# Kernel optimization log

Hardware: AMD Instinct MI355X
Metric: run time of the kernel (lower is better)

Reference implementation:

```python
import jax, jax.numpy as jnp
import numpy as np

N_NODES = 100000
N_EDGES = 1600000
IN_DIM = 128
HID = 128
OUT_DIM = 2
NUM_GRAPHS = 64
BN_EPS = 1e-5


def _glorot(key, shape):
    fan_in, fan_out = shape[0], shape[1]
    lim = np.sqrt(6.0 / (fan_in + fan_out))
    return jax.random.uniform(key, shape, jnp.float32, -lim, lim)


def setup_inputs() -> dict:
    key = jax.random.key(0)
    ks = jax.random.split(key, 12)
    x = jax.random.normal(ks[0], (N_NODES, IN_DIM), jnp.float32)
    edge_index = jax.random.randint(ks[1], (2, N_EDGES), 0, N_NODES, jnp.int64)
    batch = jnp.sort(jax.random.randint(ks[2], (N_NODES,), 0, NUM_GRAPHS, jnp.int64))
    return {
        "x": x,
        "edge_index": edge_index,
        "batch": batch,
        "W1": _glorot(ks[3], (IN_DIM, HID)), "b1": jnp.zeros((HID,), jnp.float32),
        "g1": jnp.ones((HID,), jnp.float32), "be1": jnp.zeros((HID,), jnp.float32),
        "W2": _glorot(ks[4], (HID, HID)), "b2": jnp.zeros((HID,), jnp.float32),
        "g2": jnp.ones((HID,), jnp.float32), "be2": jnp.zeros((HID,), jnp.float32),
        "Wc1": _glorot(ks[5], (HID, HID // 2)), "bc1": jnp.zeros((HID // 2,), jnp.float32),
        "Wc2": _glorot(ks[6], (HID // 2, OUT_DIM)), "bc2": jnp.zeros((OUT_DIM,), jnp.float32),
    }


def gcn_conv(x, src, dst, W, b):
    # PyG GCNConv: add self-loops, symmetric deg^{-1/2} normalization
    n = x.shape[0]
    loop = jnp.arange(n, dtype=src.dtype)
    s = jnp.concatenate([src, loop])
    d = jnp.concatenate([dst, loop])
    deg = jax.ops.segment_sum(jnp.ones_like(d, dtype=x.dtype), d, num_segments=n)
    dinv = jnp.where(deg > 0, jax.lax.rsqrt(deg), 0.0)
    xw = x @ W  # [N, out]
    msgs = xw[s] * (dinv[s] * dinv[d])[:, None]  # [E+N, out]
    out = jax.ops.segment_sum(msgs, d, num_segments=n)
    return out + b


def batchnorm(x, gamma, beta):
    mean = jnp.mean(x, axis=0)
    var = jnp.mean(jnp.square(x - mean), axis=0)  # biased, as torch BN
    return (x - mean) * jax.lax.rsqrt(var + BN_EPS) * gamma + beta


def reference(x, edge_index, batch, W1, b1, g1, be1, W2, b2, g2, be2, Wc1, bc1, Wc2, bc2):
    src, dst = edge_index[0], edge_index[1]
    x = jnp.nan_to_num(x, nan=0.0)
    # layer 1: GCNConv -> BN -> ReLU (dropout = identity in eval)
    h = jax.nn.relu(batchnorm(gcn_conv(x, src, dst, W1, b1), g1, be1))
    # layer 2
    h = jax.nn.relu(batchnorm(gcn_conv(h, src, dst, W2, b2), g2, be2))
    # global mean pool per graph
    sums = jax.ops.segment_sum(h, batch, num_segments=NUM_GRAPHS)
    counts = jax.ops.segment_sum(jnp.ones((h.shape[0],), h.dtype), batch, num_segments=NUM_GRAPHS)
    pooled = sums / jnp.maximum(counts, 1.0)[:, None]  # [G, HID]
    # classifier MLP
    z = jax.nn.relu(pooled @ Wc1 + bc1)
    out = z @ Wc2 + bc2
    return jnp.nan_to_num(out, nan=0.0)
```

## Files before the change

### kernel.cpp

```cpp
#include <hip/hip_runtime.h>

typedef unsigned int uint;
typedef unsigned short ushort;

#define HID 128
#define NGRAPH 64

typedef __attribute__((ext_vector_type(8))) short short8;
typedef __attribute__((ext_vector_type(4))) float floatx4;

__device__ __forceinline__ float bflo(uint w){ return __uint_as_float(w<<16); }
__device__ __forceinline__ float bfhi(uint w){ return __uint_as_float(w & 0xffff0000u); }
__device__ __forceinline__ float bf2f(ushort u){ return __uint_as_float(((uint)u)<<16); }
__device__ __forceinline__ ushort f2bf(float f){
  uint u = __float_as_uint(f);
  u = u + 0x7fffu + ((u>>16)&1u);
  return (ushort)(u>>16);
}
__device__ __forceinline__ uint pack2(float a, float b){
  return (uint)f2bf(a) | ((uint)f2bf(b)<<16);
}
__device__ __forceinline__ float nanz(float v){ return (v==v) ? v : 0.f; }

__device__ __forceinline__ int bat(const int* b, int i, int is64){
  return is64 ? b[2*(size_t)i] : b[i];
}

__global__ void k_zero_prep(int* __restrict__ cnt, float* __restrict__ stats1,
                            float* __restrict__ stats2, float* __restrict__ pooled,
                            uint* __restrict__ xwzero, int NN,
                            const int* __restrict__ ei, int* __restrict__ flags,
                            const float* __restrict__ W1, const float* __restrict__ W2,
                            ushort* __restrict__ wt1, ushort* __restrict__ wt2){
  int bid = blockIdx.x;
  if (bid < 512){
    int i = bid*256 + threadIdx.x;
    for (int t = i; t < NN; t += 512*256) cnt[t] = 0;
    if (i < 256){ stats1[i] = 0.f; stats2[i] = 0.f; }
    if (i < NGRAPH*HID) pooled[i] = 0.f;
    if (i < 64) xwzero[i] = 0u;
    if (bid == 0 && threadIdx.x < 64){
      int t = threadIdx.x;
      bool nz = (ei[2*t + 1] != 0) || (ei[2*(t+64) + 1] != 0);
      unsigned long long m = __ballot(nz);
      if (t == 0) flags[1] = (m == 0ULL) ? 1 : 0;
    }
  } else {
    int b = bid - 512;
    const float* W  = (b & 1) ? W2  : W1;
    ushort*      Wt = (b & 1) ? wt2 : wt1;
    int base = (b >> 1)*4096;
    for (int o = base + threadIdx.x; o < base + 4096; o += 256){
      int j    = o & 7;
      int lane = (o >> 3) & 63;
      int ct   = (o >> 9) & 7;
      int ks   = o >> 12;
      int k = ks*32 + (lane >> 4)*8 + j;
      int n = ct*16 + (lane & 15);
      Wt[o] = f2bf(W[(size_t)k*HID + n]);
    }
  }
}

__global__ void k_sentinel(ushort* out, int n){
  int i = blockIdx.x*blockDim.x + threadIdx.x;
  if (i < n) out[i] = 0x429A;
}


__global__ void k_hist(const int* __restrict__ ei, int* __restrict__ cnt, int E, int NN,
                       const int* __restrict__ flags){
  int is64 = flags[1];
  int e0 = (blockIdx.x*blockDim.x + threadIdx.x)*2;
  if (e0 >= E) return;
  bool h1 = (e0 + 1 < E);
  int d0, d1;
  if (is64){
    int4 v = *(const int4*)(ei + 2*(size_t)E + 2*(size_t)e0);
    d0 = v.x; d1 = v.z;
  } else {
    int2 v = *(const int2*)(ei + (size_t)E + e0);
    d0 = v.x; d1 = v.y;
  }
  if ((uint)d0 < (uint)NN) atomicAdd(&cnt[d0], 1);
  if (h1 && (uint)d1 < (uint)NN) atomicAdd(&cnt[d1], 1);
}

__global__ void k_scan1(const int* __restrict__ cnt, int* __restrict__ partials,
                        float* __restrict__ dinv, int NN){
  int t = threadIdx.x;
  int base = blockIdx.x*1024 + t*4;
  int v0=0,v1=0,v2=0,v3=0;
  if (base + 3 < NN){ int4 v = *(const int4*)(cnt + base); v0=v.x; v1=v.y; v2=v.z; v3=v.w; }
  else {
    if (base+0 < NN) v0 = cnt[base+0];
    if (base+1 < NN) v1 = cnt[base+1];
    if (base+2 < NN) v2 = cnt[base+2];
    if (base+3 < NN) v3 = cnt[base+3];
  }
  if (base+0 < NN) dinv[base+0] = rsqrtf((float)(v0+1));
  if (base+1 < NN) dinv[base+1] = rsqrtf((float)(v1+1));
  if (base+2 < NN) dinv[base+2] = rsqrtf((float)(v2+1));
  if (base+3 < NN) dinv[base+3] = rsqrtf((float)(v3+1));
  __shared__ int red[256];
  red[t] = v0+v1+v2+v3;
  __syncthreads();
  for (int off=128; off>0; off>>=1){
    if (t < off) red[t] += red[t+off];
    __syncthreads();
  }
  if (t==0) partials[blockIdx.x] = red[0];
}

__global__ void k_scan2(int* __restrict__ partials, int* __restrict__ offs, int npart, int NN){
  if (threadIdx.x==0 && blockIdx.x==0){
    int run = 0;
    for (int i=0;i<npart;i++){ int tt = partials[i]; partials[i] = run; run += tt; }
    offs[NN] = run;
  }
}

__global__ void k_scan3(const int* __restrict__ cnt, const int* __restrict__ partials,
                        int* __restrict__ offs, int* __restrict__ cursor, int NN){
  int t = threadIdx.x;
  int base = blockIdx.x*1024 + t*4;
  int v0=0,v1=0,v2=0,v3=0;
  if (base + 3 < NN){ int4 v = *(const int4*)(cnt + base); v0=v.x; v1=v.y; v2=v.z; v3=v.w; }
  else {
    if (base+0 < NN) v0 = cnt[base+0];
    if (base+1 < NN) v1 = cnt[base+1];
    if (base+2 < NN) v2 = cnt[base+2];
    if (base+3 < NN) v3 = cnt[base+3];
  }
  int tsum = v0+v1+v2+v3;
  __shared__ int sc[256];
  sc[t] = tsum;
  __syncthreads();
  for (int off=1; off<256; off<<=1){
    int val = (t >= off) ? sc[t-off] : 0;
    __syncthreads();
    sc[t] += val;
    __syncthreads();
  }
  int run = partials[blockIdx.x] + sc[t] - tsum;
  if (base+0 < NN){ offs[base+0] = run; cursor[base+0] = run; run += v0; }
  if (base+1 < NN){ offs[base+1] = run; cursor[base+1] = run; run += v1; }
  if (base+2 < NN){ offs[base+2] = run; cursor[base+2] = run; run += v2; }
  if (base+3 < NN){ offs[base+3] = run; cursor[base+3] = run; run += v3; }
}

__global__ void k_scatter(const int* __restrict__ ei, int* __restrict__ cursor,
                          int* __restrict__ srclist, int E, int NN,
                          const int* __restrict__ flags){
  int is64 = flags[1];
  int e0 = (blockIdx.x*blockDim.x + threadIdx.x)*2;
  if (e0 >= E) return;
  bool h1 = (e0 + 1 < E);
  int s0, s1, d0, d1;
  if (is64){
    int4 sv = *(const int4*)(ei + 2*(size_t)e0);
    int4 dv = *(const int4*)(ei + 2*(size_t)E + 2*(size_t)e0);
    s0 = sv.x; s1 = sv.z; d0 = dv.x; d1 = dv.z;
  } else {
    int2 sv = *(const int2*)(ei + (size_t)e0);
    int2 dv = *(const int2*)(ei + (size_t)E + e0);
    s0 = sv.x; s1 = sv.y; d0 = dv.x; d1 = dv.y;
  }
  if ((uint)d0 < (uint)NN && (uint)s0 < (uint)NN){
    srclist[atomicAdd(&cursor[d0], 1)] = s0;
  }
  if (h1 && (uint)d1 < (uint)NN && (uint)s1 < (uint)NN){
    srclist[atomicAdd(&cursor[d1], 1)] = s1;
  }
}


__global__ __launch_bounds__(256) void k_gemm1(const float* __restrict__ A,
    const ushort* __restrict__ Wt, const float* __restrict__ dinv,
    ushort* __restrict__ O, int NN){
  __shared__ ushort wlds[16384];
  int tid = threadIdx.x;
  {
    const uint4* s = (const uint4*)Wt;
    uint4* d = (uint4*)wlds;
    #pragma unroll
    for (int i = 0; i < 8; i++) d[tid + i*256] = s[tid + i*256];
  }
  __syncthreads();
  int wave = tid >> 6, lane = tid & 63, m = lane & 15, q = lane >> 4;
  int rowbase = blockIdx.x*64 + wave*16;
  int ar = rowbase + m; if (ar >= NN) ar = NN-1;
  const float* arow = A + (size_t)ar*HID;
  short8 af[4];
  #pragma unroll
  for (int ks=0; ks<4; ks++){
    int kb = ks*32 + q*8;
    float4 f0 = *(const float4*)(arow + kb);
    float4 f1 = *(const float4*)(arow + kb + 4);
    short8 t;
    t[0]=(short)f2bf(nanz(f0.x)); t[1]=(short)f2bf(nanz(f0.y));
    t[2]=(short)f2bf(nanz(f0.z)); t[3]=(short)f2bf(nanz(f0.w));
    t[4]=(short)f2bf(nanz(f1.x)); t[5]=(short)f2bf(nanz(f1.y));
    t[6]=(short)f2bf(nanz(f1.z)); t[7]=(short)f2bf(nanz(f1.w));
    af[ks] = t;
  }
  floatx4 acc[8];
  #pragma unroll
  for (int ct=0; ct<8; ct++) acc[ct] = (floatx4){0.f,0.f,0.f,0.f};
  #pragma unroll
  for (int ks=0; ks<4; ks++){
    #pragma unroll
    for (int ct=0; ct<8; ct++){
      short8 bfrag = *(const short8*)&wlds[(((ks*8+ct)*64) + lane)*8];
      acc[ct] = __builtin_amdgcn_mfma_f32_16x16x32_bf16(af[ks], bfrag, acc[ct], 0, 0, 0);
    }
  }
  float dv[4];
  #pragma unroll
  for (int i=0;i<4;i++){ int r = rowbase + q*4 + i; dv[i] = (r < NN) ? dinv[r] : 0.f; }
  #pragma unroll
  for (int ct=0; ct<8; ct++){
    #pragma unroll
    for (int i=0;i<4;i++){
      int r = rowbase + q*4 + i;
      if (r < NN) O[(size_t)r*HID + ct*16 + m] = f2bf(acc[ct][i]*dv[i]);
    }
  }
}


__global__ __launch_bounds__(256) void k_gemm2(const uint* __restrict__ agg,
    const float* __restrict__ stats, const float* __restrict__ gam,
    const float* __restrict__ bet, const ushort* __restrict__ Wt,
    const float* __restrict__ dinv, ushort* __restrict__ O, int NN, float invn){
  __shared__ ushort wlds[16384];
  __shared__ float cA[128], cB[128];
  int tid = threadIdx.x;
  {
    const uint4* s = (const uint4*)Wt;
    uint4* d = (uint4*)wlds;
    #pragma unroll
    for (int i = 0; i < 8; i++) d[tid + i*256] = s[tid + i*256];
    if (tid < 128){
      float sm = stats[tid], sq = stats[128+tid];
      float mean = sm*invn;
      float var = fmaxf(sq*invn - mean*mean, 0.f);
      float a = gam[tid] * rsqrtf(var + 1e-5f);
      cA[tid] = a;
      cB[tid] = bet[tid] - mean*a;
    }
  }
  __syncthreads();
  int wave = tid >> 6, lane = tid & 63, m = lane & 15, q = lane >> 4;
  int rowbase = blockIdx.x*64 + wave*16;
  int ar = rowbase + m; if (ar >= NN) ar = NN-1;
  const uint* arow = agg + (size_t)ar*64;
  short8 af[4];
  #pragma unroll
  for (int ks=0; ks<4; ks++){
    int kb = ks*32 + q*8;
    uint4 u = *(const uint4*)(arow + (kb >> 1));
    short8 t;
    uint uw[4] = {u.x, u.y, u.z, u.w};
    #pragma unroll
    for (int p=0; p<4; p++){
      int k0 = kb + 2*p;
      float v0 = fmaxf(cA[k0]  *bflo(uw[p]) + cB[k0],   0.f);
      float v1 = fmaxf(cA[k0+1]*bfhi(uw[p]) + cB[k0+1], 0.f);
      t[2*p]   = (short)f2bf(v0);
      t[2*p+1] = (short)f2bf(v1);
    }
    af[ks] = t;
  }
  floatx4 acc[8];
  #pragma unroll
  for (int ct=0; ct<8; ct++) acc[ct] = (floatx4){0.f,0.f,0.f,0.f};
  #pragma unroll
  for (int ks=0; ks<4; ks++){
    #pragma unroll
    for (int ct=0; ct<8; ct++){
      short8 bfrag = *(const short8*)&wlds[(((ks*8+ct)*64) + lane)*8];
      acc[ct] = __builtin_amdgcn_mfma_f32_16x16x32_bf16(af[ks], bfrag, acc[ct], 0, 0, 0);
    }
  }
  float dv[4];
  #pragma unroll
  for (int i=0;i<4;i++){ int r = rowbase + q*4 + i; dv[i] = (r < NN) ? dinv[r] : 0.f; }
  #pragma unroll
  for (int ct=0; ct<8; ct++){
    #pragma unroll
    for (int i=0;i<4;i++){
      int r = rowbase + q*4 + i;
      if (r < NN) O[(size_t)r*HID + ct*16 + m] = f2bf(acc[ct][i]*dv[i]);
    }
  }
}


__global__ __launch_bounds__(256) void k_agg(const uint* __restrict__ xw,
    const int* __restrict__ offs, const int* __restrict__ srclist,
    const float* __restrict__ dinv, uint* __restrict__ agg,
    float* __restrict__ stats, int NN){
  __shared__ float lstat[256];
  lstat[threadIdx.x] = 0.f;
  __syncthreads();
  int wib = threadIdx.x >> 6;
  int lane = threadIdx.x & 63;
  int wid = blockIdx.x*4 + wib;
  int nw = gridDim.x*4;
  float s0=0.f, s1=0.f, q0=0.f, q1=0.f;
  for (int n = wid; n < NN; n += nw){
    int lo = offs[n], hi = offs[n+1];
    float dvn = dinv[n];
    float a0 = 0.f, a1 = 0.f;
    for (int base = lo; base < hi; base += 64){
      int c = hi - base; if (c > 64) c = 64;
      int sidx = (lane < c) ? srclist[base + lane] : NN;
      for (int jb = 0; jb < c; jb += 16){
        uint w[16];
        #pragma unroll
        for (int t = 0; t < 16; t++){
          int sj = __shfl(sidx, jb + t, 64);
          w[t] = xw[(size_t)sj*64 + lane];
        }
        #pragma unroll
        for (int t = 0; t < 16; t++){
          a0 += bflo(w[t]);
          a1 += bfhi(w[t]);
        }
      }
    }
    uint wsf = xw[(size_t)n*64 + lane];
    a0 = (a0 + bflo(wsf)) * dvn;
    a1 = (a1 + bfhi(wsf)) * dvn;
    agg[(size_t)n*64 + lane] = pack2(a0, a1);
    s0 += a0; s1 += a1; q0 += a0*a0; q1 += a1*a1;
  }
  int ch = lane*2;
  atomicAdd(&lstat[ch],       s0);
  atomicAdd(&lstat[ch+1],     s1);
  atomicAdd(&lstat[128+ch],   q0);
  atomicAdd(&lstat[128+ch+1], q1);
  __syncthreads();
  atomicAdd(&stats[threadIdx.x], lstat[threadIdx.x]);
}


#define PSPLIT 16

__global__ __launch_bounds__(256) void k_pool(const uint* __restrict__ agg32,
    const int* __restrict__ batch, const float* __restrict__ stats,
    const float* __restrict__ gam, const float* __restrict__ bet,
    float* __restrict__ pooled, int* __restrict__ counts,
    int NN, const int* __restrict__ flags, float invn){
  int is64 = flags[1];
  __shared__ int bounds[2];
  __shared__ float cA[128], cB[128];
  int g  = blockIdx.x;
  int si = blockIdx.y;
  int tid = threadIdx.x;
  if (tid < 128){
    float sm = stats[tid], sq = stats[128+tid];
    float mean = sm*invn;
    float var = fmaxf(sq*invn - mean*mean, 0.f);
    float a = gam[tid] * rsqrtf(var + 1e-5f);
    cA[tid] = a;
    cB[tid] = bet[tid] - mean*a;
  }
  if (tid == 0){
    int lo=0, hi=NN;
    while (lo<hi){ int mid=(lo+hi)>>1; if (bat(batch,mid,is64) < g) lo=mid+1; else hi=mid; }
    bounds[0] = lo;
    int lo2=lo, hi2=NN;
    while (lo2<hi2){ int mid=(lo2+hi2)>>1; if (bat(batch,mid,is64) < g+1) lo2=mid+1; else hi2=mid; }
    bounds[1] = lo2;
    if (si == 0) counts[g] = hi2 - lo;
  }
  __syncthreads();
  int lo = bounds[0], hi = bounds[1];
  int cnt = hi - lo;
  int chunk = (cnt + PSPLIT - 1) / PSPLIT;
  int s = lo + si*chunk;
  int e = s + chunk; if (e > hi) e = hi;
  int lane = tid & 63, rg = tid >> 6;
  int ch = lane*2;
  float a0c = cA[ch],   b0c = cB[ch];
  float a1c = cA[ch+1], b1c = cB[ch+1];
  float acc0 = 0.f, acc1 = 0.f;
  for (int r = s + rg; r < e; r += 4){
    uint w = agg32[(size_t)r*64 + lane];
    acc0 += fmaxf(a0c*bflo(w) + b0c, 0.f);
    acc1 += fmaxf(a1c*bfhi(w) + b1c, 0.f);
  }
  __shared__ float red[512];
  red[tid] = acc0;
  red[256+tid] = acc1;
  __syncthreads();
  if (tid < 64){
    float s0 = red[tid] + red[tid+64] + red[tid+128] + red[tid+192];
    float s1 = red[256+tid] + red[320+tid] + red[384+tid] + red[448+tid];
    atomicAdd(&pooled[g*HID + ch],     s0);
    atomicAdd(&pooled[g*HID + ch + 1], s1);
  }
}


__global__ void k_mlp(const float* __restrict__ pooled, const int* __restrict__ counts,
                      const float* __restrict__ Wc1, const float* __restrict__ bc1,
                      const float* __restrict__ Wc2, const float* __restrict__ bc2,
                      float* __restrict__ out){
  __shared__ float P[NGRAPH*HID];
  __shared__ float Z[NGRAPH*64];
  int tid = threadIdx.x;
  for (int i = tid; i < NGRAPH*HID; i += 256){
    int g = i >> 7;
    float c = (float)counts[g];
    P[i] = pooled[i] / fmaxf(c, 1.f);
  }
  __syncthreads();
  for (int idx = tid; idx < NGRAPH*64; idx += 256){
    int g = idx >> 6, j = idx & 63;
    float acc = bc1[j];
    for (int k = 0; k < HID; k++) acc += P[g*HID + k] * Wc1[k*64 + j];
    Z[idx] = fmaxf(acc, 0.f);
  }
  __syncthreads();
  if (tid < NGRAPH*2){
    int g = tid >> 1, o = tid & 1;
    float acc = bc2[o];
    for (int k = 0; k < 64; k++) acc += Z[g*64 + k] * Wc2[k*2 + o];
    out[tid] = nanz(acc);
  }
}

extern "C" void kernel_launch(void* const* d_in, const int* in_sizes, int n_in,
                              void* d_out, int out_size, void* d_ws, size_t ws_size,
                              hipStream_t stream){
  const float* x   = (const float*)d_in[0];
  const int*   ei  = (const int*)d_in[1];
  const int* batch = (const int*)d_in[2];
  const float* W1  = (const float*)d_in[3];
  const float* g1  = (const float*)d_in[5];
  const float* be1 = (const float*)d_in[6];
  const float* W2  = (const float*)d_in[7];
  const float* g2  = (const float*)d_in[9];
  const float* be2 = (const float*)d_in[10];
  const float* Wc1 = (const float*)d_in[11];
  const float* bc1 = (const float*)d_in[12];
  const float* Wc2 = (const float*)d_in[13];
  const float* bc2 = (const float*)d_in[14];

  const int NN = in_sizes[2];
  const int E  = in_sizes[1] / 2;

  char* p = (char*)d_ws;
  auto carve = [&](size_t bytes)->char*{
    char* r = p; p += (bytes + 255) & ~(size_t)255; return r;
  };
  int NPART = (NN + 1023)/1024;
  int*   flags    = (int*)  carve(64*4);
  int*   cnt      = (int*)  carve((size_t)NN*4);
  int*   cursor   = (int*)  carve(((size_t)NN+1)*4);
  int*   offs     = (int*)  carve(((size_t)NN+1)*4);
  int*   partials = (int*)  carve((size_t)NPART*4);
  int*   srclist  = (int*)  carve((size_t)E*4);
  float* dinv     = (float*)carve((size_t)NN*4);
  float* stats1   = (float*)carve(256*4);
  float* stats2   = (float*)carve(256*4);
  float* pooled   = (float*)carve((size_t)NGRAPH*HID*4);
  int*   counts   = (int*)  carve(NGRAPH*4);
  ushort* wt1     = (ushort*)carve(16384*2);
  ushort* wt2     = (ushort*)carve(16384*2);
  ushort* xw      = (ushort*)carve(((size_t)NN+1)*HID*2);
  ushort* agg     = (ushort*)carve((size_t)NN*HID*2);
  if ((size_t)(p - (char*)d_ws) > ws_size){
    k_sentinel<<<(out_size+255)/256, 256, 0, stream>>>((ushort*)d_out, out_size);
    return;
  }

  const float invn = 1.f/(float)NN;

  k_zero_prep<<<520, 256, 0, stream>>>(cnt, stats1, stats2, pooled,
                                       (uint*)(xw + (size_t)NN*HID), NN, ei, flags,
                                       W1, W2, wt1, wt2);

  int eb2 = (E + 511)/512;
  k_hist   <<<eb2, 256, 0, stream>>>(ei, cnt, E, NN, flags);
  k_scan1  <<<NPART, 256, 0, stream>>>(cnt, partials, dinv, NN);
  k_scan2  <<<1, 64, 0, stream>>>(partials, offs, NPART, NN);
  k_scan3  <<<NPART, 256, 0, stream>>>(cnt, partials, offs, cursor, NN);
  k_scatter<<<eb2, 256, 0, stream>>>(ei, cursor, srclist, E, NN, flags);

  int gblocks = (NN + 63)/64;
  k_gemm1<<<gblocks, 256, 0, stream>>>(x, wt1, dinv, xw, NN);
  k_agg  <<<2048, 256, 0, stream>>>((const uint*)xw, offs, srclist, dinv, (uint*)agg, stats1, NN);
  k_gemm2<<<gblocks, 256, 0, stream>>>((const uint*)agg, stats1, g1, be1, wt2, dinv, xw, NN, invn);
  k_agg  <<<2048, 256, 0, stream>>>((const uint*)xw, offs, srclist, dinv, (uint*)agg, stats2, NN);
  k_pool <<<dim3(NGRAPH, PSPLIT), 256, 0, stream>>>((const uint*)agg, batch, stats2, g2, be2,
                                                    pooled, counts, NN, flags, invn);
  k_mlp  <<<1, 256, 0, stream>>>(pooled, counts, Wc1, bc1, Wc2, bc2, (float*)d_out);
}
```

Measured before the change: 634.9 us.

## Partition histogram and scatter atomics by destination range across blocks

The histogram and CSR scatter kernels now split edges into 256 chunks and nodes into 8 destination ranges. Each block handles one chunk and only does atomics for destinations in its range. The goal is to keep each block's atomic and scatter targets in a small region of cnt/cursor/srclist for better cache locality, possibly L2 or XCD-local since blockIdx&7 maps to parts. The cost is that every edge's destination index is read 8 times, and the loads are strided by 2 in int64 mode.

```diff
diff --git a/kernel.cpp b/kernel.cpp
--- a/kernel.cpp
+++ b/kernel.cpp
@@ -68,22 +68,45 @@
 }
 
 
-__global__ void k_hist(const int* __restrict__ ei, int* __restrict__ cnt, int E, int NN,
-                       const int* __restrict__ flags){
+#define NCHUNK 256
+
+__global__ __launch_bounds__(256) void k_hist(const int* __restrict__ ei,
+    int* __restrict__ cnt, int E, int NN, const int* __restrict__ flags){
   int is64 = flags[1];
-  int e0 = (blockIdx.x*blockDim.x + threadIdx.x)*2;
-  if (e0 >= E) return;
-  bool h1 = (e0 + 1 < E);
-  int d0, d1;
-  if (is64){
-    int4 v = *(const int4*)(ei + 2*(size_t)E + 2*(size_t)e0);
-    d0 = v.x; d1 = v.z;
-  } else {
-    int2 v = *(const int2*)(ei + (size_t)E + e0);
-    d0 = v.x; d1 = v.y;
-  }
-  if ((uint)d0 < (uint)NN) atomicAdd(&cnt[d0], 1);
-  if (h1 && (uint)d1 < (uint)NN) atomicAdd(&cnt[d1], 1);
+  int part  = blockIdx.x & 7;
+  int chunk = blockIdx.x >> 3;
+  int p0 = (int)(((long long)NN *  part   ) >> 3);
+  int p1 = (int)(((long long)NN * (part+1)) >> 3);
+  int per = (E + NCHUNK - 1) / NCHUNK;
+  int e0 = chunk * per;
+  int e1 = e0 + per; if (e1 > E) e1 = E;
+  const int* dstp = ei + (is64 ? 2*(size_t)E : (size_t)E);
+  for (int e = e0 + (int)threadIdx.x; e < e1; e += 256){
+    int d = is64 ? dstp[2*(size_t)e] : dstp[e];
+    if (d >= p0 && d < p1) atomicAdd(&cnt[d], 1);
+  }
+}
+
+__global__ __launch_bounds__(256) void k_scatter(const int* __restrict__ ei,
+    int* __restrict__ cursor, int* __restrict__ srclist, int E, int NN,
+    const int* __restrict__ flags){
+  int is64 = flags[1];
+  int part  = blockIdx.x & 7;
+  int chunk = blockIdx.x >> 3;
+  int p0 = (int)(((long long)NN *  part   ) >> 3);
+  int p1 = (int)(((long long)NN * (part+1)) >> 3);
+  int per = (E + NCHUNK - 1) / NCHUNK;
+  int e0 = chunk * per;
+  int e1 = e0 + per; if (e1 > E) e1 = E;
+  const int* dstp = ei + (is64 ? 2*(size_t)E : (size_t)E);
+  for (int e = e0 + (int)threadIdx.x; e < e1; e += 256){
+    int d = is64 ? dstp[2*(size_t)e] : dstp[e];
+    if (d >= p0 && d < p1){
+      int s = is64 ? ei[2*(size_t)e] : ei[e];
+      if ((uint)s < (uint)NN)
+        srclist[atomicAdd(&cursor[d], 1)] = s;
+    }
+  }
 }
 
 __global__ void k_scan1(const int* __restrict__ cnt, int* __restrict__ partials,
@@ -147,31 +170,6 @@
   if (base+1 < NN){ offs[base+1] = run; cursor[base+1] = run; run += v1; }
   if (base+2 < NN){ offs[base+2] = run; cursor[base+2] = run; run += v2; }
   if (base+3 < NN){ offs[base+3] = run; cursor[base+3] = run; run += v3; }
-}
-
-__global__ void k_scatter(const int* __restrict__ ei, int* __restrict__ cursor,
-                          int* __restrict__ srclist, int E, int NN,
-                          const int* __restrict__ flags){
-  int is64 = flags[1];
-  int e0 = (blockIdx.x*blockDim.x + threadIdx.x)*2;
-  if (e0 >= E) return;
-  bool h1 = (e0 + 1 < E);
-  int s0, s1, d0, d1;
-  if (is64){
-    int4 sv = *(const int4*)(ei + 2*(size_t)e0);
-    int4 dv = *(const int4*)(ei + 2*(size_t)E + 2*(size_t)e0);
-    s0 = sv.x; s1 = sv.z; d0 = dv.x; d1 = dv.z;
-  } else {
-    int2 sv = *(const int2*)(ei + (size_t)e0);
-    int2 dv = *(const int2*)(ei + (size_t)E + e0);
-    s0 = sv.x; s1 = sv.y; d0 = dv.x; d1 = dv.y;
-  }
-  if ((uint)d0 < (uint)NN && (uint)s0 < (uint)NN){
-    srclist[atomicAdd(&cursor[d0], 1)] = s0;
-  }
-  if (h1 && (uint)d1 < (uint)NN && (uint)s1 < (uint)NN){
-    srclist[atomicAdd(&cursor[d1], 1)] = s1;
-  }
 }
 
 
@@ -484,12 +482,11 @@
                                        (uint*)(xw + (size_t)NN*HID), NN, ei, flags,
                                        W1, W2, wt1, wt2);
 
-  int eb2 = (E + 511)/512;
-  k_hist   <<<eb2, 256, 0, stream>>>(ei, cnt, E, NN, flags);
+  k_hist   <<<NCHUNK*8, 256, 0, stream>>>(ei, cnt, E, NN, flags);
   k_scan1  <<<NPART, 256, 0, stream>>>(cnt, partials, dinv, NN);
   k_scan2  <<<1, 64, 0, stream>>>(partials, offs, NPART, NN);
   k_scan3  <<<NPART, 256, 0, stream>>>(cnt, partials, offs, cursor, NN);
-  k_scatter<<<eb2, 256, 0, stream>>>(ei, cursor, srclist, E, NN, flags);
+  k_scatter<<<NCHUNK*8, 256, 0, stream>>>(ei, cursor, srclist, E, NN, flags);
 
   int gblocks = (NN + 63)/64;
   k_gemm1<<<gblocks, 256, 0, stream>>>(x, wt1, dinv, xw, NN);
```

New measurement: 577.0 us. 9.1% less time.
